# Kernel optimization log

Hardware: AMD Instinct MI355X
Metric: run time of the kernel (lower is better)

## Reference

```python
import jax, jax.numpy as jnp
import numpy as np

# RosaAttention config constants
H = 16       # num_rosa_heads
KV = 4       # num_rosa_key_value_heads
QKB = 64     # num_rosa_query_key_bits
VB = 64      # num_rosa_value_bits
HID = 2048   # hidden_size
TAU = 1.0    # temperature buffer


def setup_inputs() -> dict:
    key = jax.random.key(0)
    ks = jax.random.split(key, 8)
    B, S = 2, 2048
    sc = 0.02
    return {
        "x": jax.random.normal(ks[0], (B, S, HID), jnp.float32),
        "attention_mask": jnp.ones((B, S), jnp.int32),
        "Wq": jax.random.normal(ks[1], (HID, H * QKB), jnp.float32) * sc,
        "Wk": jax.random.normal(ks[2], (HID, KV * QKB), jnp.float32) * sc,
        "Wv": jax.random.normal(ks[3], (HID, KV * VB), jnp.float32) * sc,
        "Wo": jax.random.normal(ks[4], (H * VB, HID), jnp.float32) * sc,
        "emb0": jnp.full((H, VB), -1e-05, jnp.float32),
        "emb1": jnp.full((H, VB), +1e-05, jnp.float32),
    }


def reference(x, attention_mask, Wq, Wk, Wv, Wo, emb0, emb1):
    B, S, _ = x.shape
    rep = H // KV
    # projections -> [b, s, heads, bits]
    xq = (x @ Wq).reshape(B, S, H, QKB)
    xk = (x @ Wk).reshape(B, S, KV, QKB)
    xv = (x @ Wv).reshape(B, S, KV, VB)
    # repeat_kv: each kv head repeated n_rep times contiguously
    xk = jnp.repeat(xk, rep, axis=2)   # [b, s, H, QKB]
    xv = jnp.repeat(xv, rep, axis=2)   # [b, s, H, VB]
    # soft bit quantization of q/k, tau-scaled bit-similarity score
    qb = jnp.tanh(xq)
    kb = jnp.tanh(xk)
    scores = jnp.einsum('bqhd,bkhd->bhqk', qb, kb) / (TAU * QKB)
    # causal mask + padding mask (mask True = attend)
    causal = jnp.tril(jnp.ones((S, S), bool))
    mask = causal[None, None] & attention_mask.astype(bool)[:, None, None, :]
    scores = jnp.where(mask, scores, jnp.finfo(scores.dtype).min)
    probs = jax.nn.softmax(scores, axis=-1)        # [b, h, q, k]
    # soft-binarized values: per-bit probabilities, attended, then mapped
    # through learned per-head bit embeddings emb0 (bit=0) / emb1 (bit=1)
    vp = jax.nn.sigmoid(xv)                        # [b, s, H, VB]
    ctx = jnp.einsum('bhqk,bkhv->bqhv', probs, vp) # [b, s, H, VB]
    out_bits = ctx * emb1[None, None] + (1.0 - ctx) * emb0[None, None]
    out = out_bits.reshape(B, S, H * VB) @ Wo      # [b, s, HID]
    return out
```

## Files before the change

kernel.cpp:

```cpp
#include <hip/hip_runtime.h>
#include <math.h>

typedef short bf16x8 __attribute__((ext_vector_type(8)));
typedef float f32x4 __attribute__((ext_vector_type(4)));
typedef float f32x16 __attribute__((ext_vector_type(16)));
typedef unsigned int u32x2 __attribute__((ext_vector_type(2)));
typedef unsigned int u32x4 __attribute__((ext_vector_type(4)));

#define MFMA_BF16(A,B,C) __builtin_amdgcn_mfma_f32_16x16x32_bf16(A,B,C,0,0,0)
#define MFMA32(A,B,C)    __builtin_amdgcn_mfma_f32_32x32x16_bf16(A,B,C,0,0,0)

#define VMCNT(N) asm volatile("s_waitcnt vmcnt(" #N ")" ::: "memory")
#define RBAR() do { asm volatile("" ::: "memory"); __builtin_amdgcn_s_barrier(); \
                    asm volatile("" ::: "memory"); } while (0)
#define PERMSWAP(a, b) asm volatile("v_permlane32_swap_b32 %0, %1" : "+v"(a), "+v"(b))

__device__ __forceinline__ unsigned short f2b(float x) {
    union { float f; unsigned int u; } v; v.f = x;
    unsigned int r = v.u + 0x7FFFu + ((v.u >> 16) & 1u);
    return (unsigned short)(r >> 16);
}

__device__ __forceinline__ unsigned int cvtpk(float lo, float hi) {
    unsigned int r;
    asm("v_cvt_pk_bf16_f32 %0, %1, %2" : "=v"(r) : "v"(lo), "v"(hi));
    return r;
}

__device__ __forceinline__ void gload16(const unsigned short* g, unsigned short* l) {
    __builtin_amdgcn_global_load_lds(
        (const __attribute__((address_space(1))) unsigned int*)(g),
        (__attribute__((address_space(3))) unsigned int*)(l),
        16, 0, 0);
}

__global__ __launch_bounds__(256) void prep(
    const float* __restrict__ x, unsigned short* __restrict__ xh,
    const float* __restrict__ Wq, const float* __restrict__ Wk,
    const float* __restrict__ Wv, unsigned short* __restrict__ Wqkvt,
    const float* __restrict__ Wo, unsigned short* __restrict__ Wot)
{
    __shared__ float t[32][33];
    const int bid = blockIdx.x, tid = threadIdx.x;

    if (bid < 2048) {
        const int n = 4096 * 2048;
        int i = bid * 256 + tid;
        int stride = 2048 * 256;
        for (int idx = i * 4; idx < n; idx += stride * 4) {
            float4 v = *(const float4*)(x + idx);
            ushort4 o;
            o.x = f2b(v.x); o.y = f2b(v.y); o.z = f2b(v.z); o.w = f2b(v.w);
            *(ushort4*)(xh + idx) = o;
        }
        return;
    }

    const int tx = tid & 31, ty = tid >> 5;

    if (bid < 5120) {
        const int idx = bid - 2048;
        const int bx = idx % 48, by = idx / 48;
        const float* src; int C, cb, dco;
        if (bx < 32)      { src = Wq; C = 1024; cb = bx;      dco = 0; }
        else if (bx < 40) { src = Wk; C = 256;  cb = bx - 32; dco = 1024; }
        else              { src = Wv; C = 256;  cb = bx - 40; dco = 1280; }
        const int c = cb * 32 + tx;
        const int r0 = by * 32;
#pragma unroll
        for (int i = 0; i < 4; ++i)
            t[ty + i * 8][tx] = src[(size_t)(r0 + ty + i * 8) * C + c];
        __syncthreads();
        const int cc = cb * 32 + ty;
#pragma unroll
        for (int i = 0; i < 4; ++i)
            Wqkvt[(size_t)(dco + cc + i * 8) * 2048 + r0 + tx] = f2b(t[tx][ty + i * 8]);
        return;
    }

    {
        const int idx = bid - 5120;
        const int bx = idx % 64, by = idx / 64;
        const int c = bx * 32 + tx;
        const int r0 = by * 32;
#pragma unroll
        for (int i = 0; i < 4; ++i)
            t[ty + i * 8][tx] = Wo[(size_t)(r0 + ty + i * 8) * 2048 + c];
        __syncthreads();
        const int cc = bx * 32 + ty;
#pragma unroll
        for (int i = 0; i < 4; ++i)
            Wot[(size_t)(cc + i * 8) * 1024 + r0 + tx] = f2b(t[tx][ty + i * 8]);
    }
}

__device__ __forceinline__ void stage_qkv(const unsigned short* AgL, const unsigned short* BgL,
                                          int K, int k0s,
                                          unsigned short* Asb, unsigned short* Bsb, int w)
{
#pragma unroll
    for (int t = 0; t < 4; ++t) {
        const int sub = t >> 1, half = t & 1;
        gload16(AgL + (size_t)(half * 16) * K + k0s + sub * 32,
                Asb + sub * 4096 + (w * 2 + half) * 512);
    }
#pragma unroll
    for (int kk = 0; kk < 2; ++kk)
        gload16(BgL + k0s + kk * 32, Bsb + kk * 2048 + w * 512);
}

__global__ __launch_bounds__(256, 3) void gemm_qkv(
    const unsigned short* __restrict__ A,
    const unsigned short* __restrict__ Bt,
    unsigned short* __restrict__ qh,
    unsigned short* __restrict__ kh,
    unsigned short* __restrict__ vtt)
{
    __shared__ __align__(16) unsigned short As[2][2 * 128 * 32];
    __shared__ __align__(16) unsigned short Bs[2][2 * 64 * 32];

    const int K = 2048;
    const int tid = threadIdx.x;
    const int w = tid >> 6, lane = tid & 63, l15 = lane & 15, quad = lane >> 4;
    const int wm = w & 1, wn = w >> 1;

    const int orig = blockIdx.x + 24 * blockIdx.y;
    const int lb = (orig & 7) * 96 + (orig >> 3);
    const int m0 = (lb / 24) * 128, n0 = (lb % 24) * 64;

    const int dsrow = lane >> 2;
    const int dscol = ((lane & 3) ^ ((lane >> 3) & 3)) * 8;
    const int sl8   = (((lane & 15) << 2) | ((lane >> 4) ^ ((lane >> 1) & 3))) * 8;

    f32x4 acc[4][2];
    const f32x4 zero4 = {0.f, 0.f, 0.f, 0.f};
#pragma unroll
    for (int i = 0; i < 4; ++i)
#pragma unroll
        for (int j = 0; j < 2; ++j) acc[i][j] = zero4;

    const unsigned short* AgL = A  + (size_t)(m0 + w * 32 + dsrow) * K + dscol;
    const unsigned short* BgL = Bt + (size_t)(n0 + w * 16 + dsrow) * K + dscol;

    const int NT = K >> 6;
    stage_qkv(AgL, BgL, K, 0, &As[0][0], &Bs[0][0], w);

    int cb = 0;
    for (int t = 0; t < NT; ++t) {
        if (t + 1 < NT) {
            stage_qkv(AgL, BgL, K, (t + 1) * 64, &As[cb ^ 1][0], &Bs[cb ^ 1][0], w);
            VMCNT(6);
        } else {
            VMCNT(0);
        }
        RBAR();

        bf16x8 af[4][2], bf[2][2];
#pragma unroll
        for (int kk = 0; kk < 2; ++kk) {
#pragma unroll
            for (int mt = 0; mt < 4; ++mt)
                af[mt][kk] = *(const bf16x8*)&As[cb][kk * 4096 + (wm * 4 + mt) * 512 + sl8];
#pragma unroll
            for (int nt = 0; nt < 2; ++nt)
                bf[nt][kk] = *(const bf16x8*)&Bs[cb][kk * 2048 + (wn * 2 + nt) * 512 + sl8];
        }
#pragma unroll
        for (int kk = 0; kk < 2; ++kk)
#pragma unroll
            for (int mt = 0; mt < 4; ++mt)
#pragma unroll
                for (int nt = 0; nt < 2; ++nt)
                    acc[mt][nt] = MFMA_BF16(af[mt][kk], bf[nt][kk], acc[mt][nt]);

        if (t + 1 < NT) RBAR();
        cb ^= 1;
    }

    if (n0 < 1024) {
#pragma unroll
        for (int mt = 0; mt < 4; ++mt)
#pragma unroll
            for (int nt = 0; nt < 2; ++nt) {
                const int gn = n0 + wn * 32 + nt * 16 + l15;
#pragma unroll
                for (int r = 0; r < 4; ++r) {
                    const int gm = m0 + wm * 64 + mt * 16 + quad * 4 + r;
                    qh[(size_t)gm * 1024 + gn] = f2b(tanhf(acc[mt][nt][r]) * 0.0225421100f);
                }
            }
    } else if (n0 < 1280) {
#pragma unroll
        for (int mt = 0; mt < 4; ++mt)
#pragma unroll
            for (int nt = 0; nt < 2; ++nt) {
                const int gn = n0 + wn * 32 + nt * 16 + l15 - 1024;
#pragma unroll
                for (int r = 0; r < 4; ++r) {
                    const int gm = m0 + wm * 64 + mt * 16 + quad * 4 + r;
                    kh[(size_t)gm * 256 + gn] = f2b(tanhf(acc[mt][nt][r]));
                }
            }
    } else {
#pragma unroll
        for (int mt = 0; mt < 4; ++mt)
#pragma unroll
            for (int nt = 0; nt < 2; ++nt) {
                const int gn = n0 + wn * 32 + nt * 16 + l15 - 1280;
                const int g = gn >> 6, vv = gn & 63;
                const int s0 = m0 + wm * 64 + mt * 16 + quad * 4;
                const int b = s0 >> 11, sl = s0 & 2047;
                ushort4 pk;
                unsigned short* pp = (unsigned short*)&pk;
#pragma unroll
                for (int r = 0; r < 4; ++r) {
                    float sv = 1.0f / (1.0f + __expf(-acc[mt][nt][r]));
                    pp[r] = f2b(sv);
                }
                *(ushort4*)&vtt[((size_t)(b * 4 + g) * 64 + vv) * 2048 + sl] = pk;
            }
    }
}

__device__ __forceinline__ void stage_out(const unsigned short* AgL, const unsigned short* BgL,
                                          int K, int k0s,
                                          unsigned short* Asb, unsigned short* Bsb, int w)
{
#pragma unroll
    for (int t = 0; t < 4; ++t) {
        const int sub = t >> 1, half = t & 1;
        gload16(AgL + (size_t)(half * 16) * K + k0s + sub * 32,
                Asb + sub * 4096 + (w * 2 + half) * 512);
        gload16(BgL + (size_t)(half * 16) * K + k0s + sub * 32,
                Bsb + sub * 4096 + (w * 2 + half) * 512);
    }
}

__global__ __launch_bounds__(256, 2) void gemm_out(
    const unsigned short* __restrict__ A,
    const unsigned short* __restrict__ Bt,
    float* __restrict__ Cf)
{
    __shared__ __align__(16) unsigned short As[2][8192];
    __shared__ __align__(16) unsigned short Bs[2][8192];

    const int K = 1024, N = 2048;
    const int tid = threadIdx.x;
    const int w = tid >> 6, lane = tid & 63, l15 = lane & 15, quad = lane >> 4;
    const int wm = w & 1, wn = w >> 1;

    const int orig = blockIdx.x + 16 * blockIdx.y;
    const int lb = (orig & 7) * 64 + (orig >> 3);
    const int m0 = (lb >> 4) * 128, n0 = (lb & 15) * 128;

    const int dsrow = lane >> 2;
    const int dscol = ((lane & 3) ^ ((lane >> 3) & 3)) * 8;
    const int sl8   = (((lane & 15) << 2) | ((lane >> 4) ^ ((lane >> 1) & 3))) * 8;

    f32x4 acc[4][4];
    const f32x4 zero4 = {0.f, 0.f, 0.f, 0.f};
#pragma unroll
    for (int i = 0; i < 4; ++i)
#pragma unroll
        for (int j = 0; j < 4; ++j) acc[i][j] = zero4;

    const unsigned short* AgL = A  + (size_t)(m0 + w * 32 + dsrow) * K + dscol;
    const unsigned short* BgL = Bt + (size_t)(n0 + w * 32 + dsrow) * K + dscol;

    const int NT = K >> 6;
    stage_out(AgL, BgL, K, 0, &As[0][0], &Bs[0][0], w);

    int cb = 0;
    for (int t = 0; t < NT; ++t) {
        if (t + 1 < NT) {
            stage_out(AgL, BgL, K, (t + 1) * 64, &As[cb ^ 1][0], &Bs[cb ^ 1][0], w);
            VMCNT(8);
        } else {
            VMCNT(0);
        }
        RBAR();

#pragma unroll
        for (int kk = 0; kk < 2; ++kk) {
            bf16x8 af[4], bf[4];
#pragma unroll
            for (int mt = 0; mt < 4; ++mt)
                af[mt] = *(const bf16x8*)&As[cb][kk * 4096 + (wm * 4 + mt) * 512 + sl8];
#pragma unroll
            for (int nt = 0; nt < 4; ++nt)
                bf[nt] = *(const bf16x8*)&Bs[cb][kk * 4096 + (wn * 4 + nt) * 512 + sl8];
#pragma unroll
            for (int mt = 0; mt < 4; ++mt)
#pragma unroll
                for (int nt = 0; nt < 4; ++nt)
                    acc[mt][nt] = MFMA_BF16(af[mt], bf[nt], acc[mt][nt]);
        }

        if (t + 1 < NT) RBAR();
        cb ^= 1;
    }

#pragma unroll
    for (int mt = 0; mt < 4; ++mt)
#pragma unroll
        for (int nt = 0; nt < 4; ++nt) {
            const int gn = n0 + wn * 64 + nt * 16 + l15;
#pragma unroll
            for (int r = 0; r < 4; ++r) {
                const int gm = m0 + wm * 64 + mt * 16 + quad * 4 + r;
                Cf[(size_t)gm * N + gn] = acc[mt][nt][r];
            }
        }
}

__global__ __launch_bounds__(256, 4) void rosa_attn_mfma(
    const unsigned short* __restrict__ qh,
    const unsigned short* __restrict__ kh,
    const unsigned short* __restrict__ vtt,
    const int* __restrict__ amask,
    const float* __restrict__ emb0,
    const float* __restrict__ emb1,
    unsigned short* __restrict__ ob)
{
    __shared__ __align__(16) unsigned short Ks[2][4096];
    __shared__ __align__(16) unsigned short Vs[2][4096];
    __shared__ unsigned int Mflg[4];
    __shared__ float Lred[2][2][32];

    const int a = blockIdx.x & 7, m = blockIdx.x >> 3;
    const int h = blockIdx.y, b = blockIdx.z, g = h >> 2;
    const int hb = h + 16 * b;
    const int sel = (m + (hb >> 3)) & 3;
    const int qt = (sel == 0) ? a : (sel == 1) ? 15 - a : (sel == 2) ? 16 + a : 31 - a;

    const int tid = threadIdx.x;
    const int w = tid >> 6, lane = tid & 63;
    const int kq = w >> 1, qq = w & 1;
    const int l31 = lane & 31, H = lane >> 5, x7 = lane & 7;

    const int srow = lane >> 3;
    const int scol = ((lane & 7) ^ srow) * 8;
    const unsigned short* kst0 = kh + ((size_t)(b * 2048) + w * 16 + srow) * 256 + g * 64 + scol;
    const unsigned short* vst0 = vtt + ((size_t)(b * 4 + g) * 64 + w * 16 + srow) * 2048 + scol;
    const int* mbase = amask + b * 2048;

    int kadr[4];
#pragma unroll
    for (int mi = 0; mi < 4; ++mi)
        kadr[mi] = (kq * 32 + l31) * 64 + (((mi * 2 + H) ^ x7) * 8);
    int vadr[2][2];
#pragma unroll
    for (int vh = 0; vh < 2; ++vh)
#pragma unroll
        for (int kc = 0; kc < 2; ++kc)
            vadr[vh][kc] = (vh * 32 + l31) * 64 + (((kq * 4 + kc * 2 + H) ^ x7) * 8);

    unsigned int cbits = 0;
#pragma unroll
    for (int r = 0; r < 16; ++r) {
        const int kl = (r & 3) + 8 * (r >> 2) + 4 * H;
        if (kl <= l31) cbits |= (1u << r);
    }

    const int q0 = qt * 64, nkt = qt + 1;

#define STAGE_TILE(k0s, buf)                                                   \
    {                                                                          \
        gload16(kst0 + (size_t)(k0s) * 256,        &Ks[buf][(w * 16) * 64]);   \
        gload16(kst0 + (size_t)(k0s) * 256 + 2048, &Ks[buf][(w * 16 + 8) * 64]);\
        gload16(vst0 + (k0s),                      &Vs[buf][(w * 16) * 64]);   \
        gload16(vst0 + (k0s) + 16384,              &Vs[buf][(w * 16 + 8) * 64]);\
    }

    const int4 mv0 = *(const int4*)(mbase + tid * 8);
    const int4 mv1 = *(const int4*)(mbase + tid * 8 + 4);

    STAGE_TILE(0, 0)

    const unsigned short* qp = qh + ((size_t)(b * 2048 + q0 + qq * 32 + l31) * 16 + h) * 64 + H * 8;
    const bf16x8 qf0 = *(const bf16x8*)(qp);
    const bf16x8 qf1 = *(const bf16x8*)(qp + 16);
    const bf16x8 qf2 = *(const bf16x8*)(qp + 32);
    const bf16x8 qf3 = *(const bf16x8*)(qp + 48);

    const bool f8 = mv0.x && mv0.y && mv0.z && mv0.w && mv1.x && mv1.y && mv1.z && mv1.w;
    const unsigned long long bal = __ballot(f8);
    const bool bytefull = ((bal >> ((lane & 7) * 8)) & 0xFFull) == 0xFFull;
    const unsigned long long bal2 = __ballot(bytefull && (lane < 8));
    if (lane == 0) Mflg[w] = (unsigned int)(bal2 & 0xFFull);
    RBAR();
    const unsigned int mflags = Mflg[0] | (Mflg[1] << 8) | (Mflg[2] << 16) | (Mflg[3] << 24);

    const f32x16 z16 = {0.f,0.f,0.f,0.f, 0.f,0.f,0.f,0.f, 0.f,0.f,0.f,0.f, 0.f,0.f,0.f,0.f};
    f32x16 oacc0 = z16, oacc1 = z16;
    float psum = 0.0f;
    const bool skipdiag = (kq > qq);

    int cb = 0;
    for (int kt = 0; kt < nkt; ++kt) {
        if (kt + 1 < nkt) {
            STAGE_TILE((kt + 1) * 64, cb ^ 1)
            VMCNT(4);
        } else {
            VMCNT(0);
        }
        RBAR();

        const bool diag = (kt == qt);
        if (!(diag && skipdiag)) {
            const bf16x8 kf0 = *(const bf16x8*)&Ks[cb][kadr[0]];
            const bf16x8 kf1 = *(const bf16x8*)&Ks[cb][kadr[1]];
            const bf16x8 kf2 = *(const bf16x8*)&Ks[cb][kadr[2]];
            const bf16x8 kf3 = *(const bf16x8*)&Ks[cb][kadr[3]];
            __builtin_amdgcn_s_setprio(1);
            f32x16 sc = MFMA32(kf0, qf0, z16);
            sc = MFMA32(kf1, qf1, sc);
            sc = MFMA32(kf2, qf2, sc);
            sc = MFMA32(kf3, qf3, sc);
            __builtin_amdgcn_s_setprio(0);

            float p[16];
#pragma unroll
            for (int r = 0; r < 16; ++r) p[r] = __builtin_exp2f(sc[r]);
            if (diag && kq == qq) {
#pragma unroll
                for (int r = 0; r < 16; ++r)
                    if (!((cbits >> r) & 1u)) p[r] = 0.0f;
            }
            if (!((mflags >> kt) & 1u)) {
#pragma unroll
                for (int r = 0; r < 16; ++r) {
                    const int kgl = kt * 64 + kq * 32 + (r & 3) + 8 * (r >> 2) + 4 * H;
                    if (mbase[kgl] == 0) p[r] = 0.0f;
                }
            }
            psum += (((p[0]+p[1])+(p[2]+p[3])) + ((p[4]+p[5])+(p[6]+p[7])))
                  + (((p[8]+p[9])+(p[10]+p[11])) + ((p[12]+p[13])+(p[14]+p[15])));

            unsigned int W0 = cvtpk(p[0],  p[1]),  W1 = cvtpk(p[2],  p[3]);
            unsigned int W2 = cvtpk(p[4],  p[5]),  W3 = cvtpk(p[6],  p[7]);
            unsigned int W4 = cvtpk(p[8],  p[9]),  W5 = cvtpk(p[10], p[11]);
            unsigned int W6 = cvtpk(p[12], p[13]), W7 = cvtpk(p[14], p[15]);
            PERMSWAP(W0, W2);  PERMSWAP(W1, W3);
            PERMSWAP(W4, W6);  PERMSWAP(W5, W7);
            u32x4 paw0; paw0[0] = W0; paw0[1] = W1; paw0[2] = W2; paw0[3] = W3;
            u32x4 paw1; paw1[0] = W4; paw1[1] = W5; paw1[2] = W6; paw1[3] = W7;
            const bf16x8 pa0 = __builtin_bit_cast(bf16x8, paw0);
            const bf16x8 pa1 = __builtin_bit_cast(bf16x8, paw1);

            const bf16x8 vb00 = *(const bf16x8*)&Vs[cb][vadr[0][0]];
            const bf16x8 vb01 = *(const bf16x8*)&Vs[cb][vadr[0][1]];
            const bf16x8 vb10 = *(const bf16x8*)&Vs[cb][vadr[1][0]];
            const bf16x8 vb11 = *(const bf16x8*)&Vs[cb][vadr[1][1]];
            __builtin_amdgcn_s_setprio(1);
            oacc0 = MFMA32(pa0, vb00, oacc0);
            oacc0 = MFMA32(pa1, vb01, oacc0);
            oacc1 = MFMA32(pa0, vb10, oacc1);
            oacc1 = MFMA32(pa1, vb11, oacc1);
            __builtin_amdgcn_s_setprio(0);
        }

        if (kt + 1 < nkt) { RBAR(); cb ^= 1; }
    }

    psum += __shfl_xor(psum, 32);

    RBAR();

    if (H == 0) Lred[kq][qq][l31] = psum;

    float* Ored = (float*)&Ks[0][0];
    const int slw = qq * 2 + (1 - kq);
    const int cx = (lane & 3) ^ ((lane >> 2) & 3);
    if (kq == 0) {
#pragma unroll
        for (int c = 0; c < 4; ++c) {
            float4 t = {oacc1[c*4+0], oacc1[c*4+1], oacc1[c*4+2], oacc1[c*4+3]};
            *(float4*)&Ored[slw * 1024 + lane * 16 + ((c ^ cx) * 4)] = t;
        }
    } else {
#pragma unroll
        for (int c = 0; c < 4; ++c) {
            float4 t = {oacc0[c*4+0], oacc0[c*4+1], oacc0[c*4+2], oacc0[c*4+3]};
            *(float4*)&Ored[slw * 1024 + lane * 16 + ((c ^ cx) * 4)] = t;
        }
    }
    RBAR();

    const int slr = qq * 2 + kq;
    f32x16 osum = (kq == 0) ? oacc0 : oacc1;
#pragma unroll
    for (int c = 0; c < 4; ++c) {
        float4 t = *(const float4*)&Ored[slr * 1024 + lane * 16 + ((c ^ cx) * 4)];
        osum[c*4+0] += t.x; osum[c*4+1] += t.y; osum[c*4+2] += t.z; osum[c*4+3] += t.w;
    }

    float rl[16];
#pragma unroll
    for (int r = 0; r < 16; ++r) {
        const int ql = (r & 3) + 8 * (r >> 2) + 4 * H;
        rl[r] = __builtin_amdgcn_rcpf(Lred[0][qq][ql] + Lred[1][qq][ql]);
    }

    const int vg = kq * 32 + l31;
    const float e0 = emb0[h * 64 + vg];
    const float ed = emb1[h * 64 + vg] - e0;
    unsigned short* obp = ob + ((size_t)(b * 2048 + q0 + qq * 32) * 16 + h) * 64 + vg;
#pragma unroll
    for (int r = 0; r < 16; ++r) {
        const int ql = (r & 3) + 8 * (r >> 2) + 4 * H;
        const float val = e0 + (osum[r] * rl[r]) * ed;
        obp[(size_t)ql * 1024] = f2b(val);
    }
#undef STAGE_TILE
}

extern "C" void kernel_launch(void* const* d_in, const int* in_sizes, int n_in,
                              void* d_out, int out_size, void* d_ws, size_t ws_size,
                              hipStream_t stream)
{
    const float* x    = (const float*)d_in[0];
    const int*   amask= (const int*)d_in[1];
    const float* Wq   = (const float*)d_in[2];
    const float* Wk   = (const float*)d_in[3];
    const float* Wv   = (const float*)d_in[4];
    const float* Wo   = (const float*)d_in[5];
    const float* emb0 = (const float*)d_in[6];
    const float* emb1 = (const float*)d_in[7];
    float* out = (float*)d_out;

    char* base = (char*)d_ws;
    unsigned short* xh    = (unsigned short*)(base);
    unsigned short* ob    = xh;
    unsigned short* Wqkvt = (unsigned short*)(base + (16u << 20));
    unsigned short* Wot   = (unsigned short*)(base + (22u << 20));
    unsigned short* qh    = (unsigned short*)(base + (26u << 20));
    unsigned short* kh    = (unsigned short*)(base + (34u << 20));
    unsigned short* vtt   = (unsigned short*)(base + (36u << 20));

    prep<<<7168, 256, 0, stream>>>(x, xh, Wq, Wk, Wv, Wqkvt, Wo, Wot);

    gemm_qkv<<<dim3(24, 32), 256, 0, stream>>>(xh, Wqkvt, qh, kh, vtt);
    rosa_attn_mfma<<<dim3(32, 16, 2), 256, 0, stream>>>(qh, kh, vtt, amask, emb0, emb1, ob);
    gemm_out<<<dim3(16, 32), 256, 0, stream>>>(ob, Wot, out);
}
```

Measured before the change: 213.9 us.

## Share K/V tiles across two query heads per 512-thread attention block

```diff
diff --git a/kernel.cpp b/kernel.cpp
--- a/kernel.cpp
+++ b/kernel.cpp
@@ -313,7 +313,7 @@
         }
 }
 
-__global__ __launch_bounds__(256, 4) void rosa_attn_mfma(
+__global__ __launch_bounds__(512, 4) void rosa_attn_mfma(
     const unsigned short* __restrict__ qh,
     const unsigned short* __restrict__ kh,
     const unsigned short* __restrict__ vtt,
@@ -322,26 +322,28 @@
     const float* __restrict__ emb1,
     unsigned short* __restrict__ ob)
 {
-    __shared__ __align__(16) unsigned short Ks[2][4096];
-    __shared__ __align__(16) unsigned short Vs[2][4096];
-    __shared__ unsigned int Mflg[4];
-    __shared__ float Lred[2][2][32];
+    __shared__ __align__(16) unsigned short KVs[16384];
+    __shared__ unsigned int Mflg[8];
+    __shared__ float Lred[2][2][2][32];
 
     const int a = blockIdx.x & 7, m = blockIdx.x >> 3;
-    const int h = blockIdx.y, b = blockIdx.z, g = h >> 2;
-    const int hb = h + 16 * b;
-    const int sel = (m + (hb >> 3)) & 3;
-    const int qt = (sel == 0) ? a : (sel == 1) ? 15 - a : (sel == 2) ? 16 + a : 31 - a;
+    const int hp = blockIdx.y, b = blockIdx.z;
+    const int g = hp >> 1, jp = hp & 1;
+    const int qt0 = (m == 0) ? a : (m == 1) ? 15 - a : (m == 2) ? 16 + a : 31 - a;
+    const int qt = b ? (31 - qt0) : qt0;
 
     const int tid = threadIdx.x;
     const int w = tid >> 6, lane = tid & 63;
-    const int kq = w >> 1, qq = w & 1;
+    const int hs = w >> 2, kq = (w >> 1) & 1, qq = w & 1;
+    const int h = g * 4 + jp * 2 + hs;
     const int l31 = lane & 31, H = lane >> 5, x7 = lane & 7;
 
     const int srow = lane >> 3;
     const int scol = ((lane & 7) ^ srow) * 8;
-    const unsigned short* kst0 = kh + ((size_t)(b * 2048) + w * 16 + srow) * 256 + g * 64 + scol;
-    const unsigned short* vst0 = vtt + ((size_t)(b * 4 + g) * 64 + w * 16 + srow) * 2048 + scol;
+    const int wr = (w & 3) * 16;
+    const bool isv = (w >= 4);
+    const unsigned short* kst0 = kh + ((size_t)(b * 2048) + wr + srow) * 256 + g * 64 + scol;
+    const unsigned short* vst0 = vtt + ((size_t)(b * 4 + g) * 64 + wr + srow) * 2048 + scol;
     const int* mbase = amask + b * 2048;
 
     int kadr[4];
@@ -353,7 +355,7 @@
     for (int vh = 0; vh < 2; ++vh)
 #pragma unroll
         for (int kc = 0; kc < 2; ++kc)
-            vadr[vh][kc] = (vh * 32 + l31) * 64 + (((kq * 4 + kc * 2 + H) ^ x7) * 8);
+            vadr[vh][kc] = 8192 + (vh * 32 + l31) * 64 + (((kq * 4 + kc * 2 + H) ^ x7) * 8);
 
     unsigned int cbits = 0;
 #pragma unroll
@@ -364,16 +366,16 @@
 
     const int q0 = qt * 64, nkt = qt + 1;
 
-#define STAGE_TILE(k0s, buf)                                                   \
-    {                                                                          \
-        gload16(kst0 + (size_t)(k0s) * 256,        &Ks[buf][(w * 16) * 64]);   \
-        gload16(kst0 + (size_t)(k0s) * 256 + 2048, &Ks[buf][(w * 16 + 8) * 64]);\
-        gload16(vst0 + (k0s),                      &Vs[buf][(w * 16) * 64]);   \
-        gload16(vst0 + (k0s) + 16384,              &Vs[buf][(w * 16 + 8) * 64]);\
-    }
-
-    const int4 mv0 = *(const int4*)(mbase + tid * 8);
-    const int4 mv1 = *(const int4*)(mbase + tid * 8 + 4);
+#define STAGE_TILE(k0s, buf)                                                        \
+    if (!isv) {                                                                     \
+        gload16(kst0 + (size_t)(k0s) * 256,        &KVs[(buf) * 4096 + wr * 64]);        \
+        gload16(kst0 + (size_t)(k0s) * 256 + 2048, &KVs[(buf) * 4096 + (wr + 8) * 64]);  \
+    } else {                                                                        \
+        gload16(vst0 + (k0s),                      &KVs[8192 + (buf) * 4096 + wr * 64]);       \
+        gload16(vst0 + (k0s) + 16384,              &KVs[8192 + (buf) * 4096 + (wr + 8) * 64]); \
+    }
+
+    const int4 mv = *(const int4*)(mbase + tid * 4);
 
     STAGE_TILE(0, 0)
 
@@ -383,13 +385,16 @@
     const bf16x8 qf2 = *(const bf16x8*)(qp + 32);
     const bf16x8 qf3 = *(const bf16x8*)(qp + 48);
 
-    const bool f8 = mv0.x && mv0.y && mv0.z && mv0.w && mv1.x && mv1.y && mv1.z && mv1.w;
+    const bool f8 = mv.x && mv.y && mv.z && mv.w;
     const unsigned long long bal = __ballot(f8);
-    const bool bytefull = ((bal >> ((lane & 7) * 8)) & 0xFFull) == 0xFFull;
-    const unsigned long long bal2 = __ballot(bytefull && (lane < 8));
-    if (lane == 0) Mflg[w] = (unsigned int)(bal2 & 0xFFull);
+    bool cf = false;
+    if (lane < 4) cf = ((bal >> (lane * 16)) & 0xFFFFull) == 0xFFFFull;
+    const unsigned int wb = (unsigned int)(__ballot((lane < 4) && cf) & 0xFull);
+    if (lane == 0) Mflg[w] = wb;
     RBAR();
-    const unsigned int mflags = Mflg[0] | (Mflg[1] << 8) | (Mflg[2] << 16) | (Mflg[3] << 24);
+    unsigned int mflags = 0;
+#pragma unroll
+    for (int i = 0; i < 8; ++i) mflags |= Mflg[i] << (i * 4);
 
     const f32x16 z16 = {0.f,0.f,0.f,0.f, 0.f,0.f,0.f,0.f, 0.f,0.f,0.f,0.f, 0.f,0.f,0.f,0.f};
     f32x16 oacc0 = z16, oacc1 = z16;
@@ -400,7 +405,7 @@
     for (int kt = 0; kt < nkt; ++kt) {
         if (kt + 1 < nkt) {
             STAGE_TILE((kt + 1) * 64, cb ^ 1)
-            VMCNT(4);
+            VMCNT(2);
         } else {
             VMCNT(0);
         }
@@ -408,10 +413,10 @@
 
         const bool diag = (kt == qt);
         if (!(diag && skipdiag)) {
-            const bf16x8 kf0 = *(const bf16x8*)&Ks[cb][kadr[0]];
-            const bf16x8 kf1 = *(const bf16x8*)&Ks[cb][kadr[1]];
-            const bf16x8 kf2 = *(const bf16x8*)&Ks[cb][kadr[2]];
-            const bf16x8 kf3 = *(const bf16x8*)&Ks[cb][kadr[3]];
+            const bf16x8 kf0 = *(const bf16x8*)&KVs[cb * 4096 + kadr[0]];
+            const bf16x8 kf1 = *(const bf16x8*)&KVs[cb * 4096 + kadr[1]];
+            const bf16x8 kf2 = *(const bf16x8*)&KVs[cb * 4096 + kadr[2]];
+            const bf16x8 kf3 = *(const bf16x8*)&KVs[cb * 4096 + kadr[3]];
             __builtin_amdgcn_s_setprio(1);
             f32x16 sc = MFMA32(kf0, qf0, z16);
             sc = MFMA32(kf1, qf1, sc);
@@ -448,10 +453,10 @@
             const bf16x8 pa0 = __builtin_bit_cast(bf16x8, paw0);
             const bf16x8 pa1 = __builtin_bit_cast(bf16x8, paw1);
 
-            const bf16x8 vb00 = *(const bf16x8*)&Vs[cb][vadr[0][0]];
-            const bf16x8 vb01 = *(const bf16x8*)&Vs[cb][vadr[0][1]];
-            const bf16x8 vb10 = *(const bf16x8*)&Vs[cb][vadr[1][0]];
-            const bf16x8 vb11 = *(const bf16x8*)&Vs[cb][vadr[1][1]];
+            const bf16x8 vb00 = *(const bf16x8*)&KVs[cb * 4096 + vadr[0][0]];
+            const bf16x8 vb01 = *(const bf16x8*)&KVs[cb * 4096 + vadr[0][1]];
+            const bf16x8 vb10 = *(const bf16x8*)&KVs[cb * 4096 + vadr[1][0]];
+            const bf16x8 vb11 = *(const bf16x8*)&KVs[cb * 4096 + vadr[1][1]];
             __builtin_amdgcn_s_setprio(1);
             oacc0 = MFMA32(pa0, vb00, oacc0);
             oacc0 = MFMA32(pa1, vb01, oacc0);
@@ -467,9 +472,9 @@
 
     RBAR();
 
-    if (H == 0) Lred[kq][qq][l31] = psum;
-
-    float* Ored = (float*)&Ks[0][0];
+    if (H == 0) Lred[hs][kq][qq][l31] = psum;
+
+    float* Ored = (float*)&KVs[0] + hs * 4096;
     const int slw = qq * 2 + (1 - kq);
     const int cx = (lane & 3) ^ ((lane >> 2) & 3);
     if (kq == 0) {
@@ -499,7 +504,7 @@
 #pragma unroll
     for (int r = 0; r < 16; ++r) {
         const int ql = (r & 3) + 8 * (r >> 2) + 4 * H;
-        rl[r] = __builtin_amdgcn_rcpf(Lred[0][qq][ql] + Lred[1][qq][ql]);
+        rl[r] = __builtin_amdgcn_rcpf(Lred[hs][0][qq][ql] + Lred[hs][1][qq][ql]);
     }
 
     const int vg = kq * 32 + l31;
@@ -541,6 +546,6 @@
     prep<<<7168, 256, 0, stream>>>(x, xh, Wq, Wk, Wv, Wqkvt, Wo, Wot);
 
     gemm_qkv<<<dim3(24, 32), 256, 0, stream>>>(xh, Wqkvt, qh, kh, vtt);
-    rosa_attn_mfma<<<dim3(32, 16, 2), 256, 0, stream>>>(qh, kh, vtt, amask, emb0, emb1, ob);
+    rosa_attn_mfma<<<dim3(32, 8, 2), 512, 0, stream>>>(qh, kh, vtt, amask, emb0, emb1, ob);
     gemm_out<<<dim3(16, 32), 256, 0, stream>>>(ob, Wot, out);
 }
```

After: 210.6 us. No clear change (-1.5%).
